# Performance work log

Measured on AMD Instinct MI355X. Metric: run time of the kernel, lower is better.

## Reference

```python
import jax, jax.numpy as jnp
import numpy as np

B, D, T = 8, 512, 2048
K = 8192


def setup_inputs() -> dict:
    key = jax.random.key(0)
    k1, k2 = jax.random.split(key)
    latents = jax.random.normal(k1, (B, D, T), dtype=jnp.float32)
    # nn.Embedding weight init: uniform(-1/K, 1/K)
    embedding = jax.random.uniform(k2, (K, D), dtype=jnp.float32,
                                   minval=-1.0 / K, maxval=1.0 / K)
    return {"latents": latents, "embedding": embedding}


def reference(latents, embedding):
    # latents: [B, D, T] -> [B, T, D]
    x = jnp.transpose(latents, (0, 2, 1))
    # squared Euclidean distances (argmin identical to cdist p=2 argmin)
    x2 = jnp.sum(x * x, axis=-1, keepdims=True)          # [B, T, 1]
    e2 = jnp.sum(embedding * embedding, axis=-1)          # [K]
    xe = jnp.einsum('btd,kd->btk', x, embedding)          # [B, T, K]
    d2 = x2 - 2.0 * xe + e2                               # [B, T, K]
    ids = jnp.argmin(d2, axis=-1)                         # [B, T] int
    quantized = embedding[ids]                            # [B, T, D] gather
    return jnp.transpose(quantized, (0, 2, 1))            # [B, D, T]
```

## Files before the change

### kernel.cpp

```cpp
#include <hip/hip_runtime.h>

#define B 8
#define D 512
#define T 2048
#define K 8192
#define M (B*T)

typedef float f32x4 __attribute__((ext_vector_type(4)));
typedef short bf16x8 __attribute__((ext_vector_type(8)));
typedef unsigned short us8 __attribute__((ext_vector_type(8)));

#define CAP_SEG 48
#define WIN 1.6e-3f

#define WS_X2    0
#define WS_E2    65536
#define WS_CNT   98304
#define WS_IDS   163840
#define WS_OVFC  229376
#define WS_OVFL  229632
#define WS_BEST  295168
#define WS_GMIN  426240
#define WS_LIST  491776
#define WS_AX    6783232
#define WS_BE    23560448
#define WS_NEED  31949056

__device__ inline unsigned short f2bf(float f) {
    unsigned int x = __float_as_uint(f);
    unsigned int r = x + 0x7fffu + ((x >> 16) & 1u);
    return (unsigned short)(r >> 16);
}

__device__ inline unsigned int f2ord(float f) {
    unsigned int u = __float_as_uint(f);
    return (u & 0x80000000u) ? ~u : (u | 0x80000000u);
}
__device__ inline float ord2f(unsigned int u) {
    return __uint_as_float((u & 0x80000000u) ? (u & 0x7fffffffu) : ~u);
}

__device__ inline void gload16(const void* g, void* l) {
    __builtin_amdgcn_global_load_lds(
        (const __attribute__((address_space(1))) unsigned int*)g,
        (__attribute__((address_space(3))) unsigned int*)l, 16, 0, 0);
}

__global__ __launch_bounds__(256)
void vq_x2_init(const float* __restrict__ lat, float* __restrict__ x2g,
                unsigned int* __restrict__ cnt_seg_u32, int* __restrict__ ovfc,
                unsigned int* __restrict__ gmin) {
#pragma clang fp contract(off)
    int p = blockIdx.x * 256 + threadIdx.x;
    cnt_seg_u32[p] = 0;
    gmin[p] = 0xFFFFFFFFu;
    if (p == 0) *ovfc = 0;
    int b = p / T, t = p % T;
    const float* base = lat + (size_t)b * D * T + t;
    float blk[4];
#pragma unroll
    for (int q = 0; q < 4; q++) {
        float r[8];
#pragma unroll
        for (int j = 0; j < 8; j++) {
            float v = base[(size_t)(q * 128 + j) * T];
            r[j] = __fmul_rn(v, v);
        }
        for (int i = 8; i < 128; i += 8) {
#pragma unroll
            for (int j = 0; j < 8; j++) {
                float v = base[(size_t)(q * 128 + i + j) * T];
                r[j] = __fadd_rn(r[j], __fmul_rn(v, v));
            }
        }
        blk[q] = __fadd_rn(__fadd_rn(__fadd_rn(r[0], r[1]), __fadd_rn(r[2], r[3])),
                           __fadd_rn(__fadd_rn(r[4], r[5]), __fadd_rn(r[6], r[7])));
    }
    x2g[p] = __fadd_rn(__fadd_rn(blk[0], blk[1]), __fadd_rn(blk[2], blk[3]));
}

__global__ __launch_bounds__(256)
void vq_x2_kernel(const float* __restrict__ lat, float* __restrict__ x2g) {
#pragma clang fp contract(off)
    int p = blockIdx.x * 256 + threadIdx.x;
    int b = p / T, t = p % T;
    const float* base = lat + (size_t)b * D * T + t;
    float blk[4];
#pragma unroll
    for (int q = 0; q < 4; q++) {
        float r[8];
#pragma unroll
        for (int j = 0; j < 8; j++) {
            float v = base[(size_t)(q * 128 + j) * T];
            r[j] = __fmul_rn(v, v);
        }
        for (int i = 8; i < 128; i += 8) {
#pragma unroll
            for (int j = 0; j < 8; j++) {
                float v = base[(size_t)(q * 128 + i + j) * T];
                r[j] = __fadd_rn(r[j], __fmul_rn(v, v));
            }
        }
        blk[q] = __fadd_rn(__fadd_rn(__fadd_rn(r[0], r[1]), __fadd_rn(r[2], r[3])),
                           __fadd_rn(__fadd_rn(r[4], r[5]), __fadd_rn(r[6], r[7])));
    }
    x2g[p] = __fadd_rn(__fadd_rn(blk[0], blk[1]), __fadd_rn(blk[2], blk[3]));
}

__global__ __launch_bounds__(256)
void vq_e2_kernel(const float* __restrict__ emb, float* __restrict__ e2g) {
#pragma clang fp contract(off)
    int k = blockIdx.x * 256 + threadIdx.x;
    const float* base = emb + (size_t)k * D;
    float blk[4];
#pragma unroll
    for (int q = 0; q < 4; q++) {
        float r[8];
        {
            float4 a = *(const float4*)&base[q * 128];
            float4 c = *(const float4*)&base[q * 128 + 4];
            r[0] = __fmul_rn(a.x, a.x); r[1] = __fmul_rn(a.y, a.y);
            r[2] = __fmul_rn(a.z, a.z); r[3] = __fmul_rn(a.w, a.w);
            r[4] = __fmul_rn(c.x, c.x); r[5] = __fmul_rn(c.y, c.y);
            r[6] = __fmul_rn(c.z, c.z); r[7] = __fmul_rn(c.w, c.w);
        }
        for (int i = 8; i < 128; i += 8) {
            float4 a = *(const float4*)&base[q * 128 + i];
            float4 c = *(const float4*)&base[q * 128 + i + 4];
            r[0] = __fadd_rn(r[0], __fmul_rn(a.x, a.x));
            r[1] = __fadd_rn(r[1], __fmul_rn(a.y, a.y));
            r[2] = __fadd_rn(r[2], __fmul_rn(a.z, a.z));
            r[3] = __fadd_rn(r[3], __fmul_rn(a.w, a.w));
            r[4] = __fadd_rn(r[4], __fmul_rn(c.x, c.x));
            r[5] = __fadd_rn(r[5], __fmul_rn(c.y, c.y));
            r[6] = __fadd_rn(r[6], __fmul_rn(c.z, c.z));
            r[7] = __fadd_rn(r[7], __fmul_rn(c.w, c.w));
        }
        blk[q] = __fadd_rn(__fadd_rn(__fadd_rn(r[0], r[1]), __fadd_rn(r[2], r[3])),
                           __fadd_rn(__fadd_rn(r[4], r[5]), __fadd_rn(r[6], r[7])));
    }
    e2g[k] = __fadd_rn(__fadd_rn(blk[0], blk[1]), __fadd_rn(blk[2], blk[3]));
}

__global__ __launch_bounds__(256)
void vq_prep_a(const float* __restrict__ lat, unsigned short* __restrict__ Ax) {
    __shared__ float xsl[64][65];
    const int tid = threadIdx.x;
    const int m0 = blockIdx.x * 64;
    const int b = m0 / T, t0 = m0 % T;
    const float* lp = lat + (size_t)b * D * T + t0;
    for (int d0 = 0; d0 < D; d0 += 64) {
        if (d0) __syncthreads();
#pragma unroll
        for (int i = 0; i < 16; i++) {
            int idx = tid + i * 256;
            int dd = idx >> 6, tt = idx & 63;
            xsl[dd][tt] = lp[(size_t)(d0 + dd) * T + tt];
        }
        __syncthreads();
        int tt = tid & 63, g = tid >> 6;
        us8 va, vb;
#pragma unroll
        for (int j = 0; j < 8; j++) va[j] = f2bf(xsl[g * 16 + j][tt]);
#pragma unroll
        for (int j = 0; j < 8; j++) vb[j] = f2bf(xsl[g * 16 + 8 + j][tt]);
        *(us8*)&Ax[(size_t)(m0 + tt) * 512 + d0 + g * 16] = va;
        *(us8*)&Ax[(size_t)(m0 + tt) * 512 + d0 + g * 16 + 8] = vb;
    }
}

__global__ __launch_bounds__(256)
void vq_prep_b(const float* __restrict__ emb, unsigned short* __restrict__ Be) {
    size_t i = ((size_t)blockIdx.x * 256 + threadIdx.x) * 4;
    float4 v = *(const float4*)&emb[i];
    ushort4 o;
    o.x = f2bf(v.x); o.y = f2bf(v.y); o.z = f2bf(v.z); o.w = f2bf(v.w);
    *(ushort4*)&Be[i] = o;
}

#define BMg 128
#define BNg 128
#define NCHUNK 2048
#define NSTEPS ((NCHUNK / BNg) * 8)

__global__ __launch_bounds__(256, 3)
void vq_gemm(const unsigned short* __restrict__ Ax,
             const unsigned short* __restrict__ Be,
             const float* __restrict__ e2g,
             unsigned int* __restrict__ gmin,
             unsigned char* __restrict__ cnt_seg,
             unsigned short* __restrict__ list) {
    __shared__ unsigned short As[BMg * 64];
    __shared__ unsigned short Bs[BNg * 64];
    __shared__ float e2s[NCHUNK];
    __shared__ int cntl[BMg];

    const int tid = threadIdx.x;
    const int lane = tid & 63;
    const int wid = tid >> 6;
    const int m0 = blockIdx.x * BMg;
    const int nc0 = blockIdx.y * NCHUNK;

    for (int i = tid; i < NCHUNK; i += 256) e2s[i] = e2g[nc0 + i];
    if (tid < BMg) cntl[tid] = 0;

    const int rbase = wid * 8 + (lane >> 3);
    const int cbyte = (((lane & 7) ^ (lane >> 3)) * 16);
    const char* gA = (const char*)Ax + (size_t)(m0 + rbase) * 1024 + cbyte;
    const char* gB = (const char*)Be + (size_t)(nc0 + rbase) * 1024 + cbyte;
    const int ldsoff = wid * 1024;

    const int rbyteA = (wid * 32 + (lane & 15)) * 128;
    const int rbyteB = ((lane & 15)) * 128;

    float runmin[2][4];
    float thrg[2][4];
#pragma unroll
    for (int mi = 0; mi < 2; mi++)
#pragma unroll
        for (int r = 0; r < 4; r++) runmin[mi][r] = 3.4e38f;

    f32x4 acc[2][8];
    for (int s = 0; s < NSTEPS; s++) {
        const int nt = s >> 3, ks = s & 7;

        __syncthreads();

        {
            const char* ga = gA + (size_t)(ks * 128);
            const char* gb = gB + (size_t)(nt * 128) * 1024 + (size_t)(ks * 128);
#pragma unroll
            for (int i = 0; i < 4; i++) {
                gload16(ga + (size_t)i * 32768, (char*)As + ldsoff + i * 4096);
                gload16(gb + (size_t)i * 32768, (char*)Bs + ldsoff + i * 4096);
            }
        }
        __syncthreads();

        if (ks == 0) {
#pragma unroll
            for (int mi = 0; mi < 2; mi++)
#pragma unroll
                for (int ni = 0; ni < 8; ni++) acc[mi][ni] = (f32x4){0.f, 0.f, 0.f, 0.f};
#pragma unroll
            for (int mi = 0; mi < 2; mi++)
#pragma unroll
                for (int r = 0; r < 4; r++) {
                    const int m = m0 + wid * 32 + mi * 16 + (lane >> 4) * 4 + r;
                    thrg[mi][r] = ord2f(gmin[m]);
                }
        }

        __builtin_amdgcn_s_setprio(1);
#pragma unroll
        for (int kh = 0; kh < 2; kh++) {
            const int cb = ((((lane >> 4) + kh * 4) ^ (lane & 7)) * 16);
            bf16x8 af[2], bfr[8];
#pragma unroll
            for (int mi = 0; mi < 2; mi++)
                af[mi] = *(const bf16x8*)((const char*)As + rbyteA + mi * 2048 + cb);
#pragma unroll
            for (int ni = 0; ni < 8; ni++)
                bfr[ni] = *(const bf16x8*)((const char*)Bs + rbyteB + ni * 2048 + cb);
#pragma unroll
            for (int mi = 0; mi < 2; mi++)
#pragma unroll
                for (int ni = 0; ni < 8; ni++)
                    acc[mi][ni] = __builtin_amdgcn_mfma_f32_16x16x32_bf16(
                        af[mi], bfr[ni], acc[mi][ni], 0, 0, 0);
        }
        __builtin_amdgcn_s_setprio(0);

        if (ks == 7) {
            const int n0l = nt * BNg;
#pragma unroll
            for (int mi = 0; mi < 2; mi++)
#pragma unroll
                for (int ni = 0; ni < 8; ni++) {
                    float e2v = e2s[n0l + ni * 16 + (lane & 15)];
#pragma unroll
                    for (int r = 0; r < 4; r++)
                        acc[mi][ni][r] = e2v - 2.0f * acc[mi][ni][r];
                }
#pragma unroll
            for (int mi = 0; mi < 2; mi++)
#pragma unroll
                for (int r = 0; r < 4; r++) {
                    float v = acc[mi][0][r];
#pragma unroll
                    for (int ni = 1; ni < 8; ni++) v = fminf(v, acc[mi][ni][r]);
                    v = fminf(v, __shfl_xor(v, 1));
                    v = fminf(v, __shfl_xor(v, 2));
                    v = fminf(v, __shfl_xor(v, 4));
                    v = fminf(v, __shfl_xor(v, 8));
                    runmin[mi][r] = fminf(runmin[mi][r], v);
                    const int rloc = wid * 32 + mi * 16 + (lane >> 4) * 4 + r;
                    const int m = m0 + rloc;
                    float th = fminf(thrg[mi][r], runmin[mi][r]) + WIN;
#pragma unroll
                    for (int ni = 0; ni < 8; ni++) {
                        if (acc[mi][ni][r] < th) {
                            int kcode = nc0 + n0l + ni * 16 + (lane & 15);
                            int slot = atomicAdd(&cntl[rloc], 1);
                            if (slot < CAP_SEG)
                                list[m * 192 + blockIdx.y * CAP_SEG + slot] =
                                    (unsigned short)kcode;
                        }
                    }
                    if ((lane & 15) == 0)
                        atomicMin(&gmin[m], f2ord(runmin[mi][r]));
                }
        }
    }

    __syncthreads();
    if (tid < BMg) {
        int c = cntl[tid];
        cnt_seg[(size_t)(m0 + tid) * 4 + blockIdx.y] =
            (unsigned char)(c > 255 ? 255 : c);
    }
}

__global__ __launch_bounds__(256)
void vq_rescore3(const float* __restrict__ lat, const float* __restrict__ emb,
                 const float* __restrict__ x2g, const float* __restrict__ e2g,
                 const unsigned char* __restrict__ cnt_seg,
                 const unsigned short* __restrict__ list,
                 int* __restrict__ ids, int* __restrict__ ovfc,
                 int* __restrict__ ovfl, unsigned long long* __restrict__ best,
                 float* __restrict__ out) {
#pragma clang fp contract(off)
    __shared__ float xs[D][32];
    __shared__ unsigned long long bests[8][32];
    __shared__ int kid_s[32];

    const int tid = threadIdx.x;
    const int w = tid >> 5;
    const int l = tid & 31;
    const int m0 = blockIdx.x * 32;
    const int b = m0 / T, t0 = m0 % T;
    const int p = m0 + l;
    const size_t lbase = (size_t)b * D * T + t0;

#pragma unroll
    for (int i = 0; i < 64; i++) {
        int idx = tid + i * 256;
        int dd = idx >> 5, tt = idx & 31;
        xs[dd][tt] = lat[lbase + (size_t)dd * T + tt];
    }

    unsigned int cs = *(const unsigned int*)&cnt_seg[(size_t)p * 4];
    int c0 = cs & 255, c1 = (cs >> 8) & 255, c2 = (cs >> 16) & 255, c3 = (cs >> 24) & 255;
    const bool ovf = (c0 > CAP_SEG) | (c1 > CAP_SEG) | (c2 > CAP_SEG) | (c3 > CAP_SEG);
    if (w == 0 && ovf) {
        int s = atomicAdd(ovfc, 1);
        ovfl[s] = p;
        best[p] = ~0ull;
    }
    __syncthreads();

    const float x2v = x2g[p];
    unsigned long long bb = ~0ull;
    if (!ovf) {
        int segc[4] = {c0, c1, c2, c3};
#pragma unroll
        for (int seg = 0; seg < 4; seg++) {
            const int c = segc[seg];
            int j = w;
            for (; j + 8 < c; j += 16) {
                int ka = list[(size_t)p * 192 + seg * CAP_SEG + j];
                int kb = list[(size_t)p * 192 + seg * CAP_SEG + j + 8];
                const float4* ea4 = (const float4*)(emb + (size_t)ka * D);
                const float4* eb4 = (const float4*)(emb + (size_t)kb * D);
                float aA = 0.f, aB = 0.f;
#pragma unroll 4
                for (int q = 0; q < D / 4; q++) {
                    float4 va = ea4[q];
                    float4 vb = eb4[q];
                    float x0 = xs[q * 4 + 0][l], x1 = xs[q * 4 + 1][l];
                    float x2_ = xs[q * 4 + 2][l], x3 = xs[q * 4 + 3][l];
                    aA = __fadd_rn(aA, __fmul_rn(x0, va.x));
                    aB = __fadd_rn(aB, __fmul_rn(x0, vb.x));
                    aA = __fadd_rn(aA, __fmul_rn(x1, va.y));
                    aB = __fadd_rn(aB, __fmul_rn(x1, vb.y));
                    aA = __fadd_rn(aA, __fmul_rn(x2_, va.z));
                    aB = __fadd_rn(aB, __fmul_rn(x2_, vb.z));
                    aA = __fadd_rn(aA, __fmul_rn(x3, va.w));
                    aB = __fadd_rn(aB, __fmul_rn(x3, vb.w));
                }
                float dA = __fadd_rn(__fsub_rn(x2v, __fadd_rn(aA, aA)), e2g[ka]);
                float dB = __fadd_rn(__fsub_rn(x2v, __fadd_rn(aB, aB)), e2g[kb]);
                unsigned long long pa = ((unsigned long long)f2ord(dA) << 32) |
                                        (unsigned long long)(unsigned int)ka;
                unsigned long long pb = ((unsigned long long)f2ord(dB) << 32) |
                                        (unsigned long long)(unsigned int)kb;
                bb = (pa < bb) ? pa : bb;
                bb = (pb < bb) ? pb : bb;
            }
            if (j < c) {
                int k = list[(size_t)p * 192 + seg * CAP_SEG + j];
                const float4* er4 = (const float4*)(emb + (size_t)k * D);
                float acc = 0.f;
#pragma unroll 4
                for (int q = 0; q < D / 4; q++) {
                    float4 e4 = er4[q];
                    acc = __fadd_rn(acc, __fmul_rn(xs[q * 4 + 0][l], e4.x));
                    acc = __fadd_rn(acc, __fmul_rn(xs[q * 4 + 1][l], e4.y));
                    acc = __fadd_rn(acc, __fmul_rn(xs[q * 4 + 2][l], e4.z));
                    acc = __fadd_rn(acc, __fmul_rn(xs[q * 4 + 3][l], e4.w));
                }
                float dist = __fadd_rn(__fsub_rn(x2v, __fadd_rn(acc, acc)), e2g[k]);
                unsigned long long pk = ((unsigned long long)f2ord(dist) << 32) |
                                        (unsigned long long)(unsigned int)k;
                bb = (pk < bb) ? pk : bb;
            }
        }
    }
    bests[w][l] = bb;
    __syncthreads();

    if (tid < 32) {
        unsigned int cs2 = *(const unsigned int*)&cnt_seg[(size_t)(m0 + tid) * 4];
        bool ov2 = ((cs2 & 255) > CAP_SEG) | (((cs2 >> 8) & 255) > CAP_SEG) |
                   (((cs2 >> 16) & 255) > CAP_SEG) | (((cs2 >> 24) & 255) > CAP_SEG);
        if (!ov2) {
            unsigned long long v = bests[0][tid];
#pragma unroll
            for (int i = 1; i < 8; i++) v = (bests[i][tid] < v) ? bests[i][tid] : v;
            int kk = (int)(v & 0xFFFFFFFFull);
            ids[m0 + tid] = kk;
            kid_s[tid] = kk;
        } else {
            kid_s[tid] = -1;
        }
    }
    __syncthreads();

    float* ebuf = &xs[0][0];
    float* outb = out + (size_t)b * D * T + t0;
    for (int d0 = 0; d0 < D; d0 += 64) {
        if (d0) __syncthreads();
#pragma unroll
        for (int i = 0; i < 8; i++) {
            int idx = tid + i * 256;
            int tt = idx >> 6, dd = idx & 63;
            int kk = kid_s[tt];
            ebuf[tt * 65 + dd] = emb[(size_t)(kk < 0 ? 0 : kk) * D + d0 + dd];
        }
        __syncthreads();
#pragma unroll
        for (int i = 0; i < 8; i++) {
            int idx = tid + i * 256;
            int tt = idx & 31, dd = idx >> 5;
            if (kid_s[tt] >= 0)
                outb[(size_t)(d0 + dd) * T + tt] = ebuf[tt * 65 + dd];
        }
    }
}

__global__ __launch_bounds__(256)
void vq_fallback_par(const float* __restrict__ lat, const float* __restrict__ emb,
                     const float* __restrict__ x2g, const float* __restrict__ e2g,
                     const int* __restrict__ ovfc, const int* __restrict__ ovfl,
                     unsigned long long* __restrict__ best) {
#pragma clang fp contract(off)
    __shared__ float xr[D];
    __shared__ unsigned long long wmin[4];
    const int n = *ovfc;
    const int ntask = n * 8;
    for (int task = blockIdx.x; task < ntask; task += gridDim.x) {
        const int m = ovfl[task >> 3];
        const int slice = task & 7;
        const int b = m / T, t = m % T;
        for (int d = threadIdx.x; d < D; d += 256)
            xr[d] = lat[(size_t)b * D * T + (size_t)d * T + t];
        __syncthreads();
        const float x2v = x2g[m];
        unsigned long long bl = ~0ull;
        for (int k = slice * 1024 + threadIdx.x; k < slice * 1024 + 1024; k += 256) {
            const float* er = emb + (size_t)k * D;
            float s = 0.f;
            for (int d = 0; d < D; d++)
                s = __fadd_rn(s, __fmul_rn(xr[d], er[d]));
            float tmp = __fsub_rn(x2v, __fadd_rn(s, s));
            float dist = __fadd_rn(tmp, e2g[k]);
            unsigned long long pk = ((unsigned long long)f2ord(dist) << 32) |
                                    (unsigned long long)(unsigned int)k;
            bl = (pk < bl) ? pk : bl;
        }
#pragma unroll
        for (int off = 1; off < 64; off <<= 1) {
            unsigned long long o = __shfl_xor(bl, off);
            bl = (o < bl) ? o : bl;
        }
        if ((threadIdx.x & 63) == 0) wmin[threadIdx.x >> 6] = bl;
        __syncthreads();
        if (threadIdx.x == 0) {
            unsigned long long v = wmin[0];
            for (int i = 1; i < 4; i++) v = (wmin[i] < v) ? wmin[i] : v;
            atomicMin(&best[m], v);
        }
        __syncthreads();
    }
}

__global__ __launch_bounds__(256)
void vq_gather_ovf(const float* __restrict__ emb, const int* __restrict__ ovfc,
                   const int* __restrict__ ovfl,
                   const unsigned long long* __restrict__ best,
                   int* __restrict__ ids, float* __restrict__ out) {
    const int n = *ovfc;
    for (int i = blockIdx.x; i < n; i += gridDim.x) {
        int m = ovfl[i];
        int b = m / T, t = m % T;
        int k = (int)(best[m] & 0xFFFFFFFFull);
        if (threadIdx.x == 0) ids[m] = k;
        for (int d = threadIdx.x; d < D; d += 256)
            out[(size_t)b * D * T + (size_t)d * T + t] = emb[(size_t)k * D + d];
    }
}

#define TM 64
#define TN 128
#define TD 32
__global__ __launch_bounds__(256)
void vq_main_old(const float* __restrict__ latents, const float* __restrict__ emb,
                 const float* __restrict__ x2g, const float* __restrict__ e2g,
                 float* __restrict__ out) {
#pragma clang fp contract(off)
    __shared__ __align__(16) float xs[TD][TM];
    __shared__ __align__(16) float es[TD][TN + 4];
    __shared__ float e2s[TN];
    __shared__ float x2s[TM];
    __shared__ int ids_s[TM];
    __shared__ __align__(16) float gbuf[64][65];
    const int tid = threadIdx.x;
    const int tn = tid & 15;
    const int tm = tid >> 4;
    const int m0 = blockIdx.x * TM;
    const int b = m0 / T;
    const int t0 = m0 % T;
    const float* lat = latents + (size_t)b * D * T + t0;
    if (tid < TM) x2s[tid] = x2g[m0 + tid];
    float minv[4];
    int mini[4];
#pragma unroll
    for (int i = 0; i < 4; i++) { minv[i] = 3.4e38f; mini[i] = 0; }
    for (int k0 = 0; k0 < K; k0 += TN) {
        __syncthreads();
        if (tid < TN) e2s[tid] = e2g[k0 + tid];
        float s[4][8];
#pragma unroll
        for (int i = 0; i < 4; i++)
#pragma unroll
            for (int j = 0; j < 8; j++) s[i][j] = 0.0f;
        for (int d0 = 0; d0 < D; d0 += TD) {
            if (d0) __syncthreads();
#pragma unroll
            for (int i = 0; i < 8; i++) {
                int idx = tid + i * 256;
                int dd = idx >> 6, tt = idx & 63;
                xs[dd][tt] = lat[(size_t)(d0 + dd) * T + tt];
            }
#pragma unroll
            for (int i = 0; i < 16; i++) {
                int idx = tid + i * 256;
                int nn = idx >> 5, dd = idx & 31;
                es[dd][nn] = emb[(size_t)(k0 + nn) * D + d0 + dd];
            }
            __syncthreads();
#pragma unroll
            for (int d = 0; d < TD; d++) {
                float4 xr = *(const float4*)&xs[d][tm * 4];
                float4 ea = *(const float4*)&es[d][tn * 4];
                float4 eb = *(const float4*)&es[d][64 + tn * 4];
                float xv[4] = {xr.x, xr.y, xr.z, xr.w};
                float ev[8] = {ea.x, ea.y, ea.z, ea.w, eb.x, eb.y, eb.z, eb.w};
#pragma unroll
                for (int i = 0; i < 4; i++)
#pragma unroll
                    for (int j = 0; j < 8; j++)
                        s[i][j] = __fadd_rn(s[i][j], __fmul_rn(xv[i], ev[j]));
            }
        }
#pragma unroll
        for (int i = 0; i < 4; i++) {
            float x2v = x2s[tm * 4 + i];
#pragma unroll
            for (int j = 0; j < 8; j++) {
                int col = (j < 4) ? (tn * 4 + j) : (64 + tn * 4 + (j - 4));
                float s2 = __fadd_rn(s[i][j], s[i][j]);
                float tmp = __fsub_rn(x2v, s2);
                float dist = __fadd_rn(tmp, e2s[col]);
                int kk = k0 + col;
                if (dist < minv[i]) { minv[i] = dist; mini[i] = kk; }
            }
        }
    }
#pragma unroll
    for (int i = 0; i < 4; i++) {
        float v1 = minv[i];
        int i1 = mini[i];
#pragma unroll
        for (int off = 1; off < 16; off <<= 1) {
            float ov = __shfl_xor(v1, off);
            int oi = __shfl_xor(i1, off);
            if (ov < v1 || (ov == v1 && oi < i1)) { v1 = ov; i1 = oi; }
        }
        if (tn == 0) ids_s[tm * 4 + i] = i1;
    }
    __syncthreads();
    float* outb = out + (size_t)b * D * T + t0;
    for (int d0 = 0; d0 < D; d0 += 64) {
        if (d0) __syncthreads();
#pragma unroll
        for (int i = 0; i < 16; i++) {
            int idx = tid + i * 256;
            int tt = idx >> 6, dd = idx & 63;
            gbuf[tt][dd] = emb[(size_t)ids_s[tt] * D + d0 + dd];
        }
        __syncthreads();
#pragma unroll
        for (int i = 0; i < 16; i++) {
            int idx = tid + i * 256;
            int dd = idx >> 6, tt = idx & 63;
            outb[(size_t)(d0 + dd) * T + tt] = gbuf[tt][dd];
        }
    }
}

extern "C" void kernel_launch(void* const* d_in, const int* in_sizes, int n_in,
                              void* d_out, int out_size, void* d_ws, size_t ws_size,
                              hipStream_t stream) {
    const float* latents = (const float*)d_in[0];
    const float* emb     = (const float*)d_in[1];
    float* out = (float*)d_out;
    char* ws = (char*)d_ws;
    float* x2g = (float*)(ws + WS_X2);
    float* e2g = (float*)(ws + WS_E2);

    if (ws_size < (size_t)WS_NEED) {
        hipLaunchKernelGGL(vq_x2_kernel, dim3(M / 256), dim3(256), 0, stream, latents, x2g);
        hipLaunchKernelGGL(vq_e2_kernel, dim3(K / 256), dim3(256), 0, stream, emb, e2g);
        hipLaunchKernelGGL(vq_main_old, dim3(M / TM), dim3(256), 0, stream,
                           latents, emb, x2g, e2g, out);
        return;
    }

    unsigned char* cnt_seg = (unsigned char*)(ws + WS_CNT);
    int* ids = (int*)(ws + WS_IDS);
    int* ovfc = (int*)(ws + WS_OVFC);
    int* ovfl = (int*)(ws + WS_OVFL);
    unsigned long long* best = (unsigned long long*)(ws + WS_BEST);
    unsigned int* gmin = (unsigned int*)(ws + WS_GMIN);
    unsigned short* list = (unsigned short*)(ws + WS_LIST);
    unsigned short* Ax = (unsigned short*)(ws + WS_AX);
    unsigned short* Be = (unsigned short*)(ws + WS_BE);

    hipLaunchKernelGGL(vq_x2_init, dim3(M / 256), dim3(256), 0, stream,
                       latents, x2g, (unsigned int*)cnt_seg, ovfc, gmin);
    hipLaunchKernelGGL(vq_e2_kernel, dim3(K / 256), dim3(256), 0, stream, emb, e2g);
    hipLaunchKernelGGL(vq_prep_a, dim3(M / 64), dim3(256), 0, stream, latents, Ax);
    hipLaunchKernelGGL(vq_prep_b, dim3((K * D) / 1024), dim3(256), 0, stream, emb, Be);
    hipLaunchKernelGGL(vq_gemm, dim3(M / BMg, K / NCHUNK), dim3(256), 0, stream,
                       Ax, Be, e2g, gmin, cnt_seg, list);
    hipLaunchKernelGGL(vq_rescore3, dim3(M / 32), dim3(256), 0, stream,
                       latents, emb, x2g, e2g, cnt_seg, list, ids, ovfc, ovfl, best, out);
    hipLaunchKernelGGL(vq_fallback_par, dim3(512), dim3(256), 0, stream,
                       latents, emb, x2g, e2g, ovfc, ovfl, best);
    hipLaunchKernelGGL(vq_gather_ovf, dim3(128), dim3(256), 0, stream,
                       emb, ovfc, ovfl, best, ids, out);
}
```

Measured before the change: 412.4 us.

## Fuse latent and codebook prep passes into two single-read kernels

Merges the x2/init pass and the bf16 transpose-conversion of the latents into one kernel. The squared norms are now computed from the shared-memory tile that the conversion already loads, so the latents are read from global memory once instead of twice. Likewise the codebook norm pass now also writes the bf16 copy, dropping a separate conversion kernel and its extra read of the embedding. The cost: the codebook kernel runs only 32 blocks with strided per-thread writes, and the x2 accumulation runs on just 64 of the 256 threads per block, so those passes may become latency bound.

```diff
diff --git a/kernel.cpp b/kernel.cpp
--- a/kernel.cpp
+++ b/kernel.cpp
@@ -47,71 +47,80 @@
 }
 
 __global__ __launch_bounds__(256)
-void vq_x2_init(const float* __restrict__ lat, float* __restrict__ x2g,
-                unsigned int* __restrict__ cnt_seg_u32, int* __restrict__ ovfc,
-                unsigned int* __restrict__ gmin) {
+void vq_prep_x(const float* __restrict__ lat, float* __restrict__ x2g,
+               unsigned short* __restrict__ Ax,
+               unsigned int* __restrict__ cnt_seg_u32, int* __restrict__ ovfc,
+               unsigned int* __restrict__ gmin) {
 #pragma clang fp contract(off)
-    int p = blockIdx.x * 256 + threadIdx.x;
-    cnt_seg_u32[p] = 0;
-    gmin[p] = 0xFFFFFFFFu;
-    if (p == 0) *ovfc = 0;
-    int b = p / T, t = p % T;
-    const float* base = lat + (size_t)b * D * T + t;
-    float blk[4];
-#pragma unroll
-    for (int q = 0; q < 4; q++) {
-        float r[8];
-#pragma unroll
-        for (int j = 0; j < 8; j++) {
-            float v = base[(size_t)(q * 128 + j) * T];
-            r[j] = __fmul_rn(v, v);
-        }
-        for (int i = 8; i < 128; i += 8) {
-#pragma unroll
-            for (int j = 0; j < 8; j++) {
-                float v = base[(size_t)(q * 128 + i + j) * T];
-                r[j] = __fadd_rn(r[j], __fmul_rn(v, v));
-            }
-        }
-        blk[q] = __fadd_rn(__fadd_rn(__fadd_rn(r[0], r[1]), __fadd_rn(r[2], r[3])),
-                           __fadd_rn(__fadd_rn(r[4], r[5]), __fadd_rn(r[6], r[7])));
-    }
-    x2g[p] = __fadd_rn(__fadd_rn(blk[0], blk[1]), __fadd_rn(blk[2], blk[3]));
+    __shared__ float xsl[64][65];
+    const int tid = threadIdx.x;
+    const int m0 = blockIdx.x * 64;
+    const int b = m0 / T, t0 = m0 % T;
+    const float* lp = lat + (size_t)b * D * T + t0;
+
+    if (tid < 64) {
+        cnt_seg_u32[m0 + tid] = 0;
+        gmin[m0 + tid] = 0xFFFFFFFFu;
+    }
+    if (blockIdx.x == 0 && tid == 0) *ovfc = 0;
+
+    float r[8], blk[4];
+#pragma unroll
+    for (int d0 = 0; d0 < D; d0 += 64) {
+        if (d0) __syncthreads();
+#pragma unroll
+        for (int i = 0; i < 16; i++) {
+            int idx = tid + i * 256;
+            int dd = idx >> 6, tt = idx & 63;
+            xsl[dd][tt] = lp[(size_t)(d0 + dd) * T + tt];
+        }
+        __syncthreads();
+        {
+            int tt = tid & 63, g = tid >> 6;
+            us8 va, vb;
+#pragma unroll
+            for (int j = 0; j < 8; j++) va[j] = f2bf(xsl[g * 16 + j][tt]);
+#pragma unroll
+            for (int j = 0; j < 8; j++) vb[j] = f2bf(xsl[g * 16 + 8 + j][tt]);
+            *(us8*)&Ax[(size_t)(m0 + tt) * 512 + d0 + g * 16] = va;
+            *(us8*)&Ax[(size_t)(m0 + tt) * 512 + d0 + g * 16 + 8] = vb;
+        }
+        if (tid < 64) {
+            if ((d0 & 64) == 0) {
+#pragma unroll
+                for (int dd = 0; dd < 8; dd++) {
+                    float v = xsl[dd][tid];
+                    r[dd] = __fmul_rn(v, v);
+                }
+#pragma unroll
+                for (int dd = 8; dd < 64; dd++) {
+                    float v = xsl[dd][tid];
+                    r[dd & 7] = __fadd_rn(r[dd & 7], __fmul_rn(v, v));
+                }
+            } else {
+#pragma unroll
+                for (int dd = 0; dd < 64; dd++) {
+                    float v = xsl[dd][tid];
+                    r[dd & 7] = __fadd_rn(r[dd & 7], __fmul_rn(v, v));
+                }
+                blk[d0 >> 7] = __fadd_rn(
+                    __fadd_rn(__fadd_rn(r[0], r[1]), __fadd_rn(r[2], r[3])),
+                    __fadd_rn(__fadd_rn(r[4], r[5]), __fadd_rn(r[6], r[7])));
+            }
+        }
+    }
+    if (tid < 64)
+        x2g[m0 + tid] = __fadd_rn(__fadd_rn(blk[0], blk[1]),
+                                  __fadd_rn(blk[2], blk[3]));
 }
 
 __global__ __launch_bounds__(256)
-void vq_x2_kernel(const float* __restrict__ lat, float* __restrict__ x2g) {
-#pragma clang fp contract(off)
-    int p = blockIdx.x * 256 + threadIdx.x;
-    int b = p / T, t = p % T;
-    const float* base = lat + (size_t)b * D * T + t;
-    float blk[4];
-#pragma unroll
-    for (int q = 0; q < 4; q++) {
-        float r[8];
-#pragma unroll
-        for (int j = 0; j < 8; j++) {
-            float v = base[(size_t)(q * 128 + j) * T];
-            r[j] = __fmul_rn(v, v);
-        }
-        for (int i = 8; i < 128; i += 8) {
-#pragma unroll
-            for (int j = 0; j < 8; j++) {
-                float v = base[(size_t)(q * 128 + i + j) * T];
-                r[j] = __fadd_rn(r[j], __fmul_rn(v, v));
-            }
-        }
-        blk[q] = __fadd_rn(__fadd_rn(__fadd_rn(r[0], r[1]), __fadd_rn(r[2], r[3])),
-                           __fadd_rn(__fadd_rn(r[4], r[5]), __fadd_rn(r[6], r[7])));
-    }
-    x2g[p] = __fadd_rn(__fadd_rn(blk[0], blk[1]), __fadd_rn(blk[2], blk[3]));
-}
-
-__global__ __launch_bounds__(256)
-void vq_e2_kernel(const float* __restrict__ emb, float* __restrict__ e2g) {
+void vq_prep_e(const float* __restrict__ emb, float* __restrict__ e2g,
+               unsigned short* __restrict__ Be) {
 #pragma clang fp contract(off)
     int k = blockIdx.x * 256 + threadIdx.x;
     const float* base = emb + (size_t)k * D;
+    unsigned short* bo = Be + (size_t)k * D;
     float blk[4];
 #pragma unroll
     for (int q = 0; q < 4; q++) {
@@ -123,6 +132,11 @@
             r[2] = __fmul_rn(a.z, a.z); r[3] = __fmul_rn(a.w, a.w);
             r[4] = __fmul_rn(c.x, c.x); r[5] = __fmul_rn(c.y, c.y);
             r[6] = __fmul_rn(c.z, c.z); r[7] = __fmul_rn(c.w, c.w);
+            ushort4 oa, oc;
+            oa.x = f2bf(a.x); oa.y = f2bf(a.y); oa.z = f2bf(a.z); oa.w = f2bf(a.w);
+            oc.x = f2bf(c.x); oc.y = f2bf(c.y); oc.z = f2bf(c.z); oc.w = f2bf(c.w);
+            *(ushort4*)&bo[q * 128] = oa;
+            *(ushort4*)&bo[q * 128 + 4] = oc;
         }
         for (int i = 8; i < 128; i += 8) {
             float4 a = *(const float4*)&base[q * 128 + i];
@@ -135,6 +149,11 @@
             r[5] = __fadd_rn(r[5], __fmul_rn(c.y, c.y));
             r[6] = __fadd_rn(r[6], __fmul_rn(c.z, c.z));
             r[7] = __fadd_rn(r[7], __fmul_rn(c.w, c.w));
+            ushort4 oa, oc;
+            oa.x = f2bf(a.x); oa.y = f2bf(a.y); oa.z = f2bf(a.z); oa.w = f2bf(a.w);
+            oc.x = f2bf(c.x); oc.y = f2bf(c.y); oc.z = f2bf(c.z); oc.w = f2bf(c.w);
+            *(ushort4*)&bo[q * 128 + i] = oa;
+            *(ushort4*)&bo[q * 128 + i + 4] = oc;
         }
         blk[q] = __fadd_rn(__fadd_rn(__fadd_rn(r[0], r[1]), __fadd_rn(r[2], r[3])),
                            __fadd_rn(__fadd_rn(r[4], r[5]), __fadd_rn(r[6], r[7])));
@@ -143,39 +162,66 @@
 }
 
 __global__ __launch_bounds__(256)
-void vq_prep_a(const float* __restrict__ lat, unsigned short* __restrict__ Ax) {
-    __shared__ float xsl[64][65];
-    const int tid = threadIdx.x;
-    const int m0 = blockIdx.x * 64;
-    const int b = m0 / T, t0 = m0 % T;
-    const float* lp = lat + (size_t)b * D * T + t0;
-    for (int d0 = 0; d0 < D; d0 += 64) {
-        if (d0) __syncthreads();
-#pragma unroll
-        for (int i = 0; i < 16; i++) {
-            int idx = tid + i * 256;
-            int dd = idx >> 6, tt = idx & 63;
-            xsl[dd][tt] = lp[(size_t)(d0 + dd) * T + tt];
-        }
-        __syncthreads();
-        int tt = tid & 63, g = tid >> 6;
-        us8 va, vb;
-#pragma unroll
-        for (int j = 0; j < 8; j++) va[j] = f2bf(xsl[g * 16 + j][tt]);
-#pragma unroll
-        for (int j = 0; j < 8; j++) vb[j] = f2bf(xsl[g * 16 + 8 + j][tt]);
-        *(us8*)&Ax[(size_t)(m0 + tt) * 512 + d0 + g * 16] = va;
-        *(us8*)&Ax[(size_t)(m0 + tt) * 512 + d0 + g * 16 + 8] = vb;
-    }
+void vq_x2_kernel(const float* __restrict__ lat, float* __restrict__ x2g) {
+#pragma clang fp contract(off)
+    int p = blockIdx.x * 256 + threadIdx.x;
+    int b = p / T, t = p % T;
+    const float* base = lat + (size_t)b * D * T + t;
+    float blk[4];
+#pragma unroll
+    for (int q = 0; q < 4; q++) {
+        float r[8];
+#pragma unroll
+        for (int j = 0; j < 8; j++) {
+            float v = base[(size_t)(q * 128 + j) * T];
+            r[j] = __fmul_rn(v, v);
+        }
+        for (int i = 8; i < 128; i += 8) {
+#pragma unroll
+            for (int j = 0; j < 8; j++) {
+                float v = base[(size_t)(q * 128 + i + j) * T];
+                r[j] = __fadd_rn(r[j], __fmul_rn(v, v));
+            }
+        }
+        blk[q] = __fadd_rn(__fadd_rn(__fadd_rn(r[0], r[1]), __fadd_rn(r[2], r[3])),
+                           __fadd_rn(__fadd_rn(r[4], r[5]), __fadd_rn(r[6], r[7])));
+    }
+    x2g[p] = __fadd_rn(__fadd_rn(blk[0], blk[1]), __fadd_rn(blk[2], blk[3]));
 }
 
 __global__ __launch_bounds__(256)
-void vq_prep_b(const float* __restrict__ emb, unsigned short* __restrict__ Be) {
-    size_t i = ((size_t)blockIdx.x * 256 + threadIdx.x) * 4;
-    float4 v = *(const float4*)&emb[i];
-    ushort4 o;
-    o.x = f2bf(v.x); o.y = f2bf(v.y); o.z = f2bf(v.z); o.w = f2bf(v.w);
-    *(ushort4*)&Be[i] = o;
+void vq_e2_kernel(const float* __restrict__ emb, float* __restrict__ e2g) {
+#pragma clang fp contract(off)
+    int k = blockIdx.x * 256 + threadIdx.x;
+    const float* base = emb + (size_t)k * D;
+    float blk[4];
+#pragma unroll
+    for (int q = 0; q < 4; q++) {
+        float r[8];
+        {
+            float4 a = *(const float4*)&base[q * 128];
+            float4 c = *(const float4*)&base[q * 128 + 4];
+            r[0] = __fmul_rn(a.x, a.x); r[1] = __fmul_rn(a.y, a.y);
+            r[2] = __fmul_rn(a.z, a.z); r[3] = __fmul_rn(a.w, a.w);
+            r[4] = __fmul_rn(c.x, c.x); r[5] = __fmul_rn(c.y, c.y);
+            r[6] = __fmul_rn(c.z, c.z); r[7] = __fmul_rn(c.w, c.w);
+        }
+        for (int i = 8; i < 128; i += 8) {
+            float4 a = *(const float4*)&base[q * 128 + i];
+            float4 c = *(const float4*)&base[q * 128 + i + 4];
+            r[0] = __fadd_rn(r[0], __fmul_rn(a.x, a.x));
+            r[1] = __fadd_rn(r[1], __fmul_rn(a.y, a.y));
+            r[2] = __fadd_rn(r[2], __fmul_rn(a.z, a.z));
+            r[3] = __fadd_rn(r[3], __fmul_rn(a.w, a.w));
+            r[4] = __fadd_rn(r[4], __fmul_rn(c.x, c.x));
+            r[5] = __fadd_rn(r[5], __fmul_rn(c.y, c.y));
+            r[6] = __fadd_rn(r[6], __fmul_rn(c.z, c.z));
+            r[7] = __fadd_rn(r[7], __fmul_rn(c.w, c.w));
+        }
+        blk[q] = __fadd_rn(__fadd_rn(__fadd_rn(r[0], r[1]), __fadd_rn(r[2], r[3])),
+                           __fadd_rn(__fadd_rn(r[4], r[5]), __fadd_rn(r[6], r[7])));
+    }
+    e2g[k] = __fadd_rn(__fadd_rn(blk[0], blk[1]), __fadd_rn(blk[2], blk[3]));
 }
 
 #define BMg 128
@@ -657,11 +703,10 @@
     unsigned short* Ax = (unsigned short*)(ws + WS_AX);
     unsigned short* Be = (unsigned short*)(ws + WS_BE);
 
-    hipLaunchKernelGGL(vq_x2_init, dim3(M / 256), dim3(256), 0, stream,
-                       latents, x2g, (unsigned int*)cnt_seg, ovfc, gmin);
-    hipLaunchKernelGGL(vq_e2_kernel, dim3(K / 256), dim3(256), 0, stream, emb, e2g);
-    hipLaunchKernelGGL(vq_prep_a, dim3(M / 64), dim3(256), 0, stream, latents, Ax);
-    hipLaunchKernelGGL(vq_prep_b, dim3((K * D) / 1024), dim3(256), 0, stream, emb, Be);
+    hipLaunchKernelGGL(vq_prep_x, dim3(M / 64), dim3(256), 0, stream,
+                       latents, x2g, Ax, (unsigned int*)cnt_seg, ovfc, gmin);
+    hipLaunchKernelGGL(vq_prep_e, dim3(K / 256), dim3(256), 0, stream,
+                       emb, e2g, Be);
     hipLaunchKernelGGL(vq_gemm, dim3(M / BMg, K / NCHUNK), dim3(256), 0, stream,
                        Ax, Be, e2g, gmin, cnt_seg, list);
     hipLaunchKernelGGL(vq_rescore3, dim3(M / 32), dim3(256), 0, stream,
```

Result: no change. 418.3 us (+1.4%).
